# Optimization experiments

Hardware: AMD Instinct MI355X
Metric: run time of the kernel (lower is better)

Reference implementation:

```python
import jax, jax.numpy as jnp
import numpy as np

B, T, C_IN, CH, NRC, ED, NL, K = 16, 4096, 165, 256, 32, 64, 4, 512


def conv1x1(x, w, b):
    # x: [B,T,Cin], w: [Cout,Cin], b: [Cout]  (kernel-size-1 Conv1d == per-timestep matmul)
    return jnp.einsum('btc,oc->bto', x, w) + b


def resblock(x, wa, ba, wb, bb):
    h = jax.nn.relu(x)
    h = jax.nn.relu(conv1x1(h, wa, ba))
    h = conv1x1(h, wb, bb)
    return x + h


def quantize_level(res, embed):
    # res: [B,T,D], embed: [D,K]
    D = res.shape[-1]
    flat = res.reshape(-1, D)  # [N,D]
    dist = (flat * flat).sum(1, keepdims=True) - 2.0 * (flat @ embed) + (embed * embed).sum(0, keepdims=True)  # [N,K]
    ind = jnp.argmin(dist, axis=1)
    q = jnp.take(embed.T, ind, axis=0).reshape(res.shape)  # codebook gather
    diff = jnp.mean(jnp.square(jax.lax.stop_gradient(q) - res))
    q_st = res + jax.lax.stop_gradient(q - res)  # straight-through
    return q_st, diff


def _p(key, shape, fan_in):
    return jax.random.normal(key, shape, dtype=jnp.float32) / np.sqrt(fan_in)


def setup_inputs() -> dict:
    key = jax.random.key(0)
    ks = jax.random.split(key, 32)
    d = {
        'x': jax.random.normal(ks[0], (B, T, C_IN), dtype=jnp.float32),
        'enc_w1': _p(ks[1], (CH // 2, C_IN), C_IN), 'enc_b1': jnp.zeros((CH // 2,), jnp.float32),
        'enc_w2': _p(ks[2], (CH, CH // 2), CH // 2), 'enc_b2': jnp.zeros((CH,), jnp.float32),
        'enc_w3': _p(ks[3], (CH, CH), CH), 'enc_b3': jnp.zeros((CH,), jnp.float32),
        'enc_res_wa': _p(ks[4], (2, NRC, CH), CH), 'enc_res_ba': jnp.zeros((2, NRC), jnp.float32),
        'enc_res_wb': _p(ks[5], (2, CH, NRC), NRC), 'enc_res_bb': jnp.zeros((2, CH), jnp.float32),
        # quantize_conv: Conv(256->64)
        'q_w': _p(ks[6], (ED, CH), CH), 'q_b': jnp.zeros((ED,), jnp.float32),
        # 4 codebooks [D,K] (torch.randn init)
        'embeds': jax.random.normal(ks[7], (NL, ED, K), dtype=jnp.float32),
        'dec_w1': _p(ks[8], (CH, ED), ED), 'dec_b1': jnp.zeros((CH,), jnp.float32),
        'dec_res_wa': _p(ks[9], (2, NRC, CH), CH), 'dec_res_ba': jnp.zeros((2, NRC), jnp.float32),
        'dec_res_wb': _p(ks[10], (2, CH, NRC), NRC), 'dec_res_bb': jnp.zeros((2, CH), jnp.float32),
        'dec_w2': _p(ks[11], (CH // 2, CH), CH), 'dec_b2': jnp.zeros((CH // 2,), jnp.float32),
        'dec_w3': _p(ks[12], (C_IN, CH // 2), CH // 2), 'dec_b3': jnp.zeros((C_IN,), jnp.float32),
    }
    return d


def reference(x, enc_w1, enc_b1, enc_w2, enc_b2, enc_w3, enc_b3,
              enc_res_wa, enc_res_ba, enc_res_wb, enc_res_bb,
              q_w, q_b, embeds,
              dec_w1, dec_b1, dec_res_wa, dec_res_ba, dec_res_wb, dec_res_bb,
              dec_w2, dec_b2, dec_w3, dec_b3):
    # work entirely in [B,T,C] layout (transposes in the torch code cancel)
    h = jax.nn.relu(conv1x1(x, enc_w1, enc_b1))
    h = jax.nn.relu(conv1x1(h, enc_w2, enc_b2))
    h = conv1x1(h, enc_w3, enc_b3)
    for i in range(2):
        h = resblock(h, enc_res_wa[i], enc_res_ba[i], enc_res_wb[i], enc_res_bb[i])
    h = jax.nn.relu(h)
    quant = conv1x1(h, q_w, q_b)  # [B,T,64]

    residual = quant
    diffs = []
    main_q = None
    for i in range(NL):
        q, d = quantize_level(residual, embeds[i])
        diffs.append(d)
        residual = residual - q
        if i == 0:
            main_q = q
    diff = jnp.mean(jnp.stack(diffs))[None]  # shape [1]

    d = conv1x1(main_q, dec_w1, dec_b1)
    for i in range(2):
        d = resblock(d, dec_res_wa[i], dec_res_ba[i], dec_res_wb[i], dec_res_bb[i])
    d = jax.nn.relu(d)
    d = jax.nn.relu(conv1x1(d, dec_w2, dec_b2))
    d = conv1x1(d, dec_w3, dec_b3)  # [B,T,165]
    return d, diff
```

## Files before the change

### kernel.cpp

```cpp
#include <hip/hip_runtime.h>

#define NROWS 65536
#define SB 256

__device__ __forceinline__ float frelu(float v) { return fmaxf(v, 0.f); }

#define OFF_WT1   0
#define OFF_WT2   21504
#define OFF_WT3   54272
#define OFF_WTQ   119808
#define OFF_WTD1  136192
#define OFF_WTD2  152576
#define OFF_WTD3  185344
#define OFF_WAPE  218112
#define OFF_WBTE  234496
#define OFF_WAPD  250880
#define OFF_WBTD  267264
#define OFF_ETG   283648
#define OFF_EN2   414720
#define OFF_DSUM  416768
#define PREP_N    416769

__global__ void prep_k(const float* __restrict__ ew1, const float* __restrict__ ew2,
                       const float* __restrict__ ew3, const float* __restrict__ qw,
                       const float* __restrict__ dw1, const float* __restrict__ dw2,
                       const float* __restrict__ dw3, const float* __restrict__ ewa,
                       const float* __restrict__ ewb, const float* __restrict__ dwa,
                       const float* __restrict__ dwb, const float* __restrict__ embeds,
                       float* __restrict__ W) {
  int idx = blockIdx.x * 256 + threadIdx.x;
  if (idx < 21504) {
    int k = idx >> 7, o = idx & 127;
    W[OFF_WT1 + idx] = (k < 165) ? ew1[o * 165 + k] : 0.f;
    return;
  }
  idx -= 21504;
  if (idx < 32768) {
    int k = idx >> 8, o = idx & 255;
    W[OFF_WT2 + idx] = ew2[o * 128 + k];
    return;
  }
  idx -= 32768;
  if (idx < 65536) {
    int k = idx >> 8, o = idx & 255;
    W[OFF_WT3 + idx] = ew3[o * 256 + k];
    return;
  }
  idx -= 65536;
  if (idx < 16384) {
    int k = idx >> 6, o = idx & 63;
    W[OFF_WTQ + idx] = qw[o * 256 + k];
    return;
  }
  idx -= 16384;
  if (idx < 16384) {
    int k = idx >> 8, o = idx & 255;
    W[OFF_WTD1 + idx] = dw1[o * 64 + k];
    return;
  }
  idx -= 16384;
  if (idx < 32768) {
    int k = idx >> 7, o = idx & 127;
    W[OFF_WTD2 + idx] = dw2[o * 256 + k];
    return;
  }
  idx -= 32768;
  if (idx < 32768) {
    int k = idx >> 8, o = idx & 255;
    W[OFF_WTD3 + idx] = (o < 165) ? dw3[o * 128 + k] : 0.f;
    return;
  }
  idx -= 32768;
  if (idx < 16384) {
    int l = idx >> 13, rem = idx & 8191;
    int k4 = rem >> 7, rem2 = rem & 127, o = rem2 >> 2, kk = rem2 & 3;
    W[OFF_WAPE + idx] = ewa[l * 8192 + o * 256 + k4 * 4 + kk];
    return;
  }
  idx -= 16384;
  if (idx < 16384) {
    int l = idx >> 13, rem = idx & 8191;
    int k = rem >> 8, o = rem & 255;
    W[OFF_WBTE + idx] = ewb[l * 8192 + o * 32 + k];
    return;
  }
  idx -= 16384;
  if (idx < 16384) {
    int l = idx >> 13, rem = idx & 8191;
    int k4 = rem >> 7, rem2 = rem & 127, o = rem2 >> 2, kk = rem2 & 3;
    W[OFF_WAPD + idx] = dwa[l * 8192 + o * 256 + k4 * 4 + kk];
    return;
  }
  idx -= 16384;
  if (idx < 16384) {
    int l = idx >> 13, rem = idx & 8191;
    int k = rem >> 8, o = rem & 255;
    W[OFF_WBTD + idx] = dwb[l * 8192 + o * 32 + k];
    return;
  }
  idx -= 16384;
  if (idx < 131072) {
    int d = idx & 63, k = (idx >> 6) & 511, l = idx >> 15;
    W[OFF_ETG + idx] = embeds[(l * 64 + d) * 512 + k];
    return;
  }
  idx -= 131072;
  if (idx < 2048) {
    int l = idx >> 9, k = idx & 511;
    float s = 0.f;
    for (int d = 0; d < 64; ++d) {
      float e = embeds[(l * 64 + d) * 512 + k];
      s = fmaf(e, e, s);
    }
    W[OFF_EN2 + idx] = s;
    return;
  }
  idx -= 2048;
  if (idx == 0) W[OFF_DSUM] = 0.f;
}

template <int CIN, int CINP, int COUT, int CP, int INSTRIDE, int OUTSTRIDE, bool RELU_IN,
          bool RELU_OUT>
__global__ __launch_bounds__(256, 4) void conv2_k(const float* in, const float* __restrict__ wT,
                                                  const float* __restrict__ b, float* out) {
  constexpr int COUTP = 64 * CP;
  constexpr bool GUARD = (COUT != COUTP);
  typedef float vCP __attribute__((ext_vector_type(CP)));
  __shared__ float xs[32][CINP];
  const int tid = threadIdx.x, lane = tid & 63, wv = tid >> 6;
  const long row0 = (long)blockIdx.x * 32;

  for (int i = tid; i < 32 * CINP; i += 256) {
    const int r = i / CINP, c = i % CINP;
    float v = (CIN == CINP || c < CIN) ? in[(row0 + r) * (long)INSTRIDE + c] : 0.f;
    if (RELU_IN) v = frelu(v);
    xs[r][c] = v;
  }
  __syncthreads();

  float acc[8][CP];
#pragma unroll
  for (int i = 0; i < 8; ++i)
#pragma unroll
    for (int j = 0; j < CP; ++j) acc[i][j] = 0.f;

  const float* wbase = wT + lane * CP;
#pragma unroll 4
  for (int k0 = 0; k0 < CINP; k0 += 4) {
    vCP wk[4];
#pragma unroll
    for (int kk = 0; kk < 4; ++kk) wk[kk] = *(const vCP*)(wbase + (k0 + kk) * COUTP);
#pragma unroll
    for (int rj = 0; rj < 8; ++rj) {
      const float4 x = *(const float4*)(&xs[wv * 8 + rj][k0]);
#pragma unroll
      for (int j = 0; j < CP; ++j) {
        acc[rj][j] = fmaf(x.x, wk[0][j], acc[rj][j]);
        acc[rj][j] = fmaf(x.y, wk[1][j], acc[rj][j]);
        acc[rj][j] = fmaf(x.z, wk[2][j], acc[rj][j]);
        acc[rj][j] = fmaf(x.w, wk[3][j], acc[rj][j]);
      }
    }
  }

  float bias[CP];
#pragma unroll
  for (int j = 0; j < CP; ++j) {
    const int o = lane * CP + j;
    bias[j] = (!GUARD || o < COUT) ? b[o] : 0.f;
  }
#pragma unroll
  for (int rj = 0; rj < 8; ++rj) {
    const long rbase = (row0 + wv * 8 + rj) * (long)OUTSTRIDE;
    if constexpr (!GUARD) {
      vCP v;
#pragma unroll
      for (int j = 0; j < CP; ++j) {
        const float t = acc[rj][j] + bias[j];
        v[j] = RELU_OUT ? frelu(t) : t;
      }
      *(vCP*)(out + rbase + lane * CP) = v;
    } else {
#pragma unroll
      for (int j = 0; j < CP; ++j) {
        const int o = lane * CP + j;
        if (o < COUT) {
          const float t = acc[rj][j] + bias[j];
          out[rbase + o] = RELU_OUT ? frelu(t) : t;
        }
      }
    }
  }
}

__global__ __launch_bounds__(512, 4) void resblock_pair_k(
    float* xbuf, const float* __restrict__ waP, const float* __restrict__ ba,
    const float* __restrict__ wbT, const float* __restrict__ bb) {
  __shared__ float wls[8192];
  __shared__ float ts[64][36];
  const int tid = threadIdx.x, lane = tid & 63, wv = tid >> 6;
  const long row0 = (long)blockIdx.x * 64;
  const int o32 = lane & 31, rh = lane >> 5;

  for (int li = 0; li < 2; ++li) {
    __syncthreads();
    for (int i = tid; i < 8192; i += 512) wls[i] = waP[li * 8192 + i];
    __syncthreads();

    {
      float a0 = 0.f, a1 = 0.f, a2 = 0.f, a3 = 0.f;
      const float* xrow = xbuf + (row0 + wv * 8 + rh * 4) * (long)SB;
#pragma unroll 4
      for (int k0 = 0; k0 < 256; k0 += 4) {
        const float4 wq = *(const float4*)(&wls[k0 * 32 + o32 * 4]);
        const float4 x0 = *(const float4*)(xrow + 0 * SB + k0);
        const float4 x1 = *(const float4*)(xrow + 1 * SB + k0);
        const float4 x2 = *(const float4*)(xrow + 2 * SB + k0);
        const float4 x3 = *(const float4*)(xrow + 3 * SB + k0);
        a0 = fmaf(frelu(x0.x), wq.x, a0);
        a0 = fmaf(frelu(x0.y), wq.y, a0);
        a0 = fmaf(frelu(x0.z), wq.z, a0);
        a0 = fmaf(frelu(x0.w), wq.w, a0);
        a1 = fmaf(frelu(x1.x), wq.x, a1);
        a1 = fmaf(frelu(x1.y), wq.y, a1);
        a1 = fmaf(frelu(x1.z), wq.z, a1);
        a1 = fmaf(frelu(x1.w), wq.w, a1);
        a2 = fmaf(frelu(x2.x), wq.x, a2);
        a2 = fmaf(frelu(x2.y), wq.y, a2);
        a2 = fmaf(frelu(x2.z), wq.z, a2);
        a2 = fmaf(frelu(x2.w), wq.w, a2);
        a3 = fmaf(frelu(x3.x), wq.x, a3);
        a3 = fmaf(frelu(x3.y), wq.y, a3);
        a3 = fmaf(frelu(x3.z), wq.z, a3);
        a3 = fmaf(frelu(x3.w), wq.w, a3);
      }
      const float bal = ba[li * 32 + o32];
      const int rB = wv * 8 + rh * 4;
      ts[rB + 0][o32] = frelu(a0 + bal);
      ts[rB + 1][o32] = frelu(a1 + bal);
      ts[rB + 2][o32] = frelu(a2 + bal);
      ts[rB + 3][o32] = frelu(a3 + bal);
    }

    __syncthreads();
    for (int i = tid; i < 8192; i += 512) wls[i] = wbT[li * 8192 + i];
    __syncthreads();

    float acc2[8][4];
#pragma unroll
    for (int i = 0; i < 8; ++i)
#pragma unroll
      for (int j = 0; j < 4; ++j) acc2[i][j] = 0.f;

#pragma unroll
    for (int k0 = 0; k0 < 32; k0 += 4) {
      const float4 wk0 = *(const float4*)(&wls[(k0 + 0) * 256 + lane * 4]);
      const float4 wk1 = *(const float4*)(&wls[(k0 + 1) * 256 + lane * 4]);
      const float4 wk2 = *(const float4*)(&wls[(k0 + 2) * 256 + lane * 4]);
      const float4 wk3 = *(const float4*)(&wls[(k0 + 3) * 256 + lane * 4]);
#pragma unroll
      for (int rj = 0; rj < 8; ++rj) {
        const float4 t4 = *(const float4*)(&ts[wv * 8 + rj][k0]);
        acc2[rj][0] = fmaf(t4.x, wk0.x, acc2[rj][0]);
        acc2[rj][1] = fmaf(t4.x, wk0.y, acc2[rj][1]);
        acc2[rj][2] = fmaf(t4.x, wk0.z, acc2[rj][2]);
        acc2[rj][3] = fmaf(t4.x, wk0.w, acc2[rj][3]);
        acc2[rj][0] = fmaf(t4.y, wk1.x, acc2[rj][0]);
        acc2[rj][1] = fmaf(t4.y, wk1.y, acc2[rj][1]);
        acc2[rj][2] = fmaf(t4.y, wk1.z, acc2[rj][2]);
        acc2[rj][3] = fmaf(t4.y, wk1.w, acc2[rj][3]);
        acc2[rj][0] = fmaf(t4.z, wk2.x, acc2[rj][0]);
        acc2[rj][1] = fmaf(t4.z, wk2.y, acc2[rj][1]);
        acc2[rj][2] = fmaf(t4.z, wk2.z, acc2[rj][2]);
        acc2[rj][3] = fmaf(t4.z, wk2.w, acc2[rj][3]);
        acc2[rj][0] = fmaf(t4.w, wk3.x, acc2[rj][0]);
        acc2[rj][1] = fmaf(t4.w, wk3.y, acc2[rj][1]);
        acc2[rj][2] = fmaf(t4.w, wk3.z, acc2[rj][2]);
        acc2[rj][3] = fmaf(t4.w, wk3.w, acc2[rj][3]);
      }
    }
    const float4 bbv = *(const float4*)(bb + li * 256 + lane * 4);
#pragma unroll
    for (int rj = 0; rj < 8; ++rj) {
      float* xp = xbuf + (row0 + wv * 8 + rj) * (long)SB + lane * 4;
      const float4 xv = *(const float4*)xp;
      float4 nv;
      nv.x = xv.x + acc2[rj][0] + bbv.x;
      nv.y = xv.y + acc2[rj][1] + bbv.y;
      nv.z = xv.z + acc2[rj][2] + bbv.z;
      nv.w = xv.w + acc2[rj][3] + bbv.w;
      *(float4*)xp = nv;
    }
  }
}

__global__ __launch_bounds__(256, 4) void vq_k(float* buf, const float* __restrict__ embeds,
                                               const float* __restrict__ en2,
                                               const float* __restrict__ etg,
                                               float* __restrict__ dsum) {
  __shared__ float resL[32][68];
  const int tid = threadIdx.x;
  const int lane = tid & 63;
  const int wv = tid >> 6;
  const long row0 = (long)blockIdx.x * 32;

  for (int rj = 0; rj < 8; ++rj) {
    const int r = wv * 8 + rj;
    resL[r][lane] = buf[(row0 + r) * (long)SB + lane];
  }

  float dloc = 0.f;

  for (int l = 0; l < 4; ++l) {
    float best[8];
    int bk[8];
#pragma unroll
    for (int i = 0; i < 8; ++i) {
      best[i] = 3.4e38f;
      bk[i] = 0;
    }

    for (int kc = 0; kc < 2; ++kc) {
      float acc[8][4];
#pragma unroll
      for (int i = 0; i < 8; ++i)
#pragma unroll
        for (int j = 0; j < 4; ++j) acc[i][j] = 0.f;

      const float* eb = embeds + ((long)l << 15) + (kc << 8) + lane * 4;
#pragma unroll 2
      for (int dq = 0; dq < 16; ++dq) {
        float4 x4[8];
#pragma unroll
        for (int rj = 0; rj < 8; ++rj) x4[rj] = *(const float4*)(&resL[wv * 8 + rj][dq * 4]);
#pragma unroll
        for (int dd = 0; dd < 4; ++dd) {
          const float4 e4 = *(const float4*)(eb + ((dq * 4 + dd) << 9));
#pragma unroll
          for (int rj = 0; rj < 8; ++rj) {
            const float xv = dd == 0 ? x4[rj].x : dd == 1 ? x4[rj].y : dd == 2 ? x4[rj].z : x4[rj].w;
            acc[rj][0] = fmaf(xv, e4.x, acc[rj][0]);
            acc[rj][1] = fmaf(xv, e4.y, acc[rj][1]);
            acc[rj][2] = fmaf(xv, e4.z, acc[rj][2]);
            acc[rj][3] = fmaf(xv, e4.w, acc[rj][3]);
          }
        }
      }

      const float4 e2 = *(const float4*)(en2 + l * 512 + kc * 256 + lane * 4);
#pragma unroll
      for (int rj = 0; rj < 8; ++rj) {
#pragma unroll
        for (int j = 0; j < 4; ++j) {
          const float ev = j == 0 ? e2.x : j == 1 ? e2.y : j == 2 ? e2.z : e2.w;
          const float s = fmaf(-2.f, acc[rj][j], ev);
          const int k = kc * 256 + lane * 4 + j;
          if (s < best[rj]) {
            best[rj] = s;
            bk[rj] = k;
          }
        }
      }
    }

#pragma unroll
    for (int rj = 0; rj < 8; ++rj) {
      float bv = best[rj];
      int bi = bk[rj];
#pragma unroll
      for (int m = 1; m < 64; m <<= 1) {
        const float ov = __shfl_xor(bv, m, 64);
        const int ok = __shfl_xor(bi, m, 64);
        if (ov < bv || (ov == bv && ok < bi)) {
          bv = ov;
          bi = ok;
        }
      }
      bk[rj] = bi;
    }

#pragma unroll
    for (int rj = 0; rj < 8; ++rj) {
      const int r = wv * 8 + rj;
      const float q = etg[((long)((l << 9) + bk[rj])) * 64 + lane];
      const float res = resL[r][lane];
      const float t = q - res;
      const float qst = res + t;
      dloc = fmaf(t, t, dloc);
      resL[r][lane] = res - qst;
      if (l == 0) buf[(row0 + r) * (long)SB + lane] = qst;
    }
  }

#pragma unroll
  for (int m = 1; m < 64; m <<= 1) dloc += __shfl_xor(dloc, m, 64);
  if (lane == 0) atomicAdd(dsum, dloc);
}

__global__ void finalize_k(const float* __restrict__ dsum, float* __restrict__ out) {
  if (threadIdx.x == 0 && blockIdx.x == 0)
    out[0] = *dsum * (1.0f / (4.0f * 65536.0f * 64.0f));
}

extern "C" void kernel_launch(void* const* d_in, const int* in_sizes, int n_in, void* d_out,
                              int out_size, void* d_ws, size_t ws_size, hipStream_t stream) {
  (void)in_sizes; (void)n_in; (void)out_size; (void)ws_size;
  const float* x = (const float*)d_in[0];
  const float* enc_w1 = (const float*)d_in[1];
  const float* enc_b1 = (const float*)d_in[2];
  const float* enc_w2 = (const float*)d_in[3];
  const float* enc_b2 = (const float*)d_in[4];
  const float* enc_w3 = (const float*)d_in[5];
  const float* enc_b3 = (const float*)d_in[6];
  const float* enc_res_wa = (const float*)d_in[7];
  const float* enc_res_ba = (const float*)d_in[8];
  const float* enc_res_wb = (const float*)d_in[9];
  const float* enc_res_bb = (const float*)d_in[10];
  const float* q_w = (const float*)d_in[11];
  const float* q_b = (const float*)d_in[12];
  const float* embeds = (const float*)d_in[13];
  const float* dec_w1 = (const float*)d_in[14];
  const float* dec_b1 = (const float*)d_in[15];
  const float* dec_res_wa = (const float*)d_in[16];
  const float* dec_res_ba = (const float*)d_in[17];
  const float* dec_res_wb = (const float*)d_in[18];
  const float* dec_res_bb = (const float*)d_in[19];
  const float* dec_w2 = (const float*)d_in[20];
  const float* dec_b2 = (const float*)d_in[21];
  const float* dec_w3 = (const float*)d_in[22];
  const float* dec_b3 = (const float*)d_in[23];

  float* ws = (float*)d_ws;
  float* buf = ws;
  float* W = ws + (long)NROWS * SB;

  float* dout = (float*)d_out;

  prep_k<<<(PREP_N + 255) / 256, 256, 0, stream>>>(enc_w1, enc_w2, enc_w3, q_w, dec_w1, dec_w2,
                                                   dec_w3, enc_res_wa, enc_res_wb, dec_res_wa,
                                                   dec_res_wb, embeds, W);

  const int GB = NROWS / 32;
  const int GR = NROWS / 64;

  conv2_k<165, 168, 128, 2, 165, SB, false, true><<<GB, 256, 0, stream>>>(x, W + OFF_WT1, enc_b1, buf);
  conv2_k<128, 128, 256, 4, SB, SB, false, true><<<GB, 256, 0, stream>>>(buf, W + OFF_WT2, enc_b2, buf);
  conv2_k<256, 256, 256, 4, SB, SB, false, false><<<GB, 256, 0, stream>>>(buf, W + OFF_WT3, enc_b3, buf);
  resblock_pair_k<<<GR, 512, 0, stream>>>(buf, W + OFF_WAPE, enc_res_ba, W + OFF_WBTE, enc_res_bb);
  conv2_k<256, 256, 64, 1, SB, SB, true, false><<<GB, 256, 0, stream>>>(buf, W + OFF_WTQ, q_b, buf);

  vq_k<<<GB, 256, 0, stream>>>(buf, embeds, W + OFF_EN2, W + OFF_ETG, W + OFF_DSUM);

  conv2_k<64, 64, 256, 4, SB, SB, false, false><<<GB, 256, 0, stream>>>(buf, W + OFF_WTD1, dec_b1, buf);
  resblock_pair_k<<<GR, 512, 0, stream>>>(buf, W + OFF_WAPD, dec_res_ba, W + OFF_WBTD, dec_res_bb);
  conv2_k<256, 256, 128, 2, SB, SB, true, true><<<GB, 256, 0, stream>>>(buf, W + OFF_WTD2, dec_b2, buf);
  conv2_k<128, 128, 165, 4, SB, 165, false, false><<<GB, 256, 0, stream>>>(buf, W + OFF_WTD3, dec_b3, dout);

  finalize_k<<<1, 64, 0, stream>>>(W + OFF_DSUM, dout + (long)NROWS * 165);
}
```

Baseline: 1.234 ms.

## Enlarge VQ register tile to 16 rows x 8 codes per thread

The VQ distance kernel now gives each block 64 rows instead of 32. Each thread computes a 16-row by 8-code accumulator tile covering all 512 codes in a single pass, instead of two 256-code passes over an 8x4 tile. This means more FMAs per codebook load and per LDS read, and the two-pass loop with its repeated residual reloads goes away. In exchange, the 128 accumulators raise register pressure: launch bounds drop to 2 blocks per CU and the grid halves, which lowers occupancy and may cause spills.

```diff
diff --git a/kernel.cpp b/kernel.cpp
--- a/kernel.cpp
+++ b/kernel.cpp
@@ -294,77 +294,115 @@
   }
 }
 
-__global__ __launch_bounds__(256, 4) void vq_k(float* buf, const float* __restrict__ embeds,
+__global__ __launch_bounds__(256, 2) void vq_k(float* buf, const float* __restrict__ embeds,
                                                const float* __restrict__ en2,
                                                const float* __restrict__ etg,
                                                float* __restrict__ dsum) {
-  __shared__ float resL[32][68];
+  __shared__ float resL[64][68];
   const int tid = threadIdx.x;
   const int lane = tid & 63;
   const int wv = tid >> 6;
-  const long row0 = (long)blockIdx.x * 32;
-
-  for (int rj = 0; rj < 8; ++rj) {
-    const int r = wv * 8 + rj;
+  const long row0 = (long)blockIdx.x * 64;
+
+#pragma unroll
+  for (int rj = 0; rj < 16; ++rj) {
+    const int r = wv * 16 + rj;
     resL[r][lane] = buf[(row0 + r) * (long)SB + lane];
   }
 
   float dloc = 0.f;
 
   for (int l = 0; l < 4; ++l) {
-    float best[8];
-    int bk[8];
-#pragma unroll
-    for (int i = 0; i < 8; ++i) {
+    float best[16];
+    int bk[16];
+#pragma unroll
+    for (int i = 0; i < 16; ++i) {
       best[i] = 3.4e38f;
       bk[i] = 0;
     }
 
-    for (int kc = 0; kc < 2; ++kc) {
-      float acc[8][4];
-#pragma unroll
-      for (int i = 0; i < 8; ++i)
-#pragma unroll
-        for (int j = 0; j < 4; ++j) acc[i][j] = 0.f;
-
-      const float* eb = embeds + ((long)l << 15) + (kc << 8) + lane * 4;
+    float acc[16][8];
+#pragma unroll
+    for (int i = 0; i < 16; ++i)
+#pragma unroll
+      for (int j = 0; j < 8; ++j) acc[i][j] = 0.f;
+
+    const float* eb0 = embeds + ((long)l << 15) + lane * 4;
+    const float* eb1 = eb0 + 256;
+
 #pragma unroll 2
-      for (int dq = 0; dq < 16; ++dq) {
-        float4 x4[8];
-#pragma unroll
-        for (int rj = 0; rj < 8; ++rj) x4[rj] = *(const float4*)(&resL[wv * 8 + rj][dq * 4]);
-#pragma unroll
-        for (int dd = 0; dd < 4; ++dd) {
-          const float4 e4 = *(const float4*)(eb + ((dq * 4 + dd) << 9));
-#pragma unroll
-          for (int rj = 0; rj < 8; ++rj) {
-            const float xv = dd == 0 ? x4[rj].x : dd == 1 ? x4[rj].y : dd == 2 ? x4[rj].z : x4[rj].w;
-            acc[rj][0] = fmaf(xv, e4.x, acc[rj][0]);
-            acc[rj][1] = fmaf(xv, e4.y, acc[rj][1]);
-            acc[rj][2] = fmaf(xv, e4.z, acc[rj][2]);
-            acc[rj][3] = fmaf(xv, e4.w, acc[rj][3]);
-          }
-        }
-      }
-
-      const float4 e2 = *(const float4*)(en2 + l * 512 + kc * 256 + lane * 4);
-#pragma unroll
-      for (int rj = 0; rj < 8; ++rj) {
-#pragma unroll
-        for (int j = 0; j < 4; ++j) {
-          const float ev = j == 0 ? e2.x : j == 1 ? e2.y : j == 2 ? e2.z : e2.w;
-          const float s = fmaf(-2.f, acc[rj][j], ev);
-          const int k = kc * 256 + lane * 4 + j;
-          if (s < best[rj]) {
-            best[rj] = s;
-            bk[rj] = k;
-          }
-        }
-      }
-    }
-
-#pragma unroll
-    for (int rj = 0; rj < 8; ++rj) {
+    for (int dq = 0; dq < 16; ++dq) {
+      const float4 ea0 = *(const float4*)(eb0 + ((dq * 4 + 0) << 9));
+      const float4 ea1 = *(const float4*)(eb0 + ((dq * 4 + 1) << 9));
+      const float4 ea2 = *(const float4*)(eb0 + ((dq * 4 + 2) << 9));
+      const float4 ea3 = *(const float4*)(eb0 + ((dq * 4 + 3) << 9));
+      const float4 eb0v = *(const float4*)(eb1 + ((dq * 4 + 0) << 9));
+      const float4 eb1v = *(const float4*)(eb1 + ((dq * 4 + 1) << 9));
+      const float4 eb2v = *(const float4*)(eb1 + ((dq * 4 + 2) << 9));
+      const float4 eb3v = *(const float4*)(eb1 + ((dq * 4 + 3) << 9));
+#pragma unroll
+      for (int rj = 0; rj < 16; ++rj) {
+        const float4 x = *(const float4*)(&resL[wv * 16 + rj][dq * 4]);
+        acc[rj][0] = fmaf(x.x, ea0.x, acc[rj][0]);
+        acc[rj][1] = fmaf(x.x, ea0.y, acc[rj][1]);
+        acc[rj][2] = fmaf(x.x, ea0.z, acc[rj][2]);
+        acc[rj][3] = fmaf(x.x, ea0.w, acc[rj][3]);
+        acc[rj][4] = fmaf(x.x, eb0v.x, acc[rj][4]);
+        acc[rj][5] = fmaf(x.x, eb0v.y, acc[rj][5]);
+        acc[rj][6] = fmaf(x.x, eb0v.z, acc[rj][6]);
+        acc[rj][7] = fmaf(x.x, eb0v.w, acc[rj][7]);
+        acc[rj][0] = fmaf(x.y, ea1.x, acc[rj][0]);
+        acc[rj][1] = fmaf(x.y, ea1.y, acc[rj][1]);
+        acc[rj][2] = fmaf(x.y, ea1.z, acc[rj][2]);
+        acc[rj][3] = fmaf(x.y, ea1.w, acc[rj][3]);
+        acc[rj][4] = fmaf(x.y, eb1v.x, acc[rj][4]);
+        acc[rj][5] = fmaf(x.y, eb1v.y, acc[rj][5]);
+        acc[rj][6] = fmaf(x.y, eb1v.z, acc[rj][6]);
+        acc[rj][7] = fmaf(x.y, eb1v.w, acc[rj][7]);
+        acc[rj][0] = fmaf(x.z, ea2.x, acc[rj][0]);
+        acc[rj][1] = fmaf(x.z, ea2.y, acc[rj][1]);
+        acc[rj][2] = fmaf(x.z, ea2.z, acc[rj][2]);
+        acc[rj][3] = fmaf(x.z, ea2.w, acc[rj][3]);
+        acc[rj][4] = fmaf(x.z, eb2v.x, acc[rj][4]);
+        acc[rj][5] = fmaf(x.z, eb2v.y, acc[rj][5]);
+        acc[rj][6] = fmaf(x.z, eb2v.z, acc[rj][6]);
+        acc[rj][7] = fmaf(x.z, eb2v.w, acc[rj][7]);
+        acc[rj][0] = fmaf(x.w, ea3.x, acc[rj][0]);
+        acc[rj][1] = fmaf(x.w, ea3.y, acc[rj][1]);
+        acc[rj][2] = fmaf(x.w, ea3.z, acc[rj][2]);
+        acc[rj][3] = fmaf(x.w, ea3.w, acc[rj][3]);
+        acc[rj][4] = fmaf(x.w, eb3v.x, acc[rj][4]);
+        acc[rj][5] = fmaf(x.w, eb3v.y, acc[rj][5]);
+        acc[rj][6] = fmaf(x.w, eb3v.z, acc[rj][6]);
+        acc[rj][7] = fmaf(x.w, eb3v.w, acc[rj][7]);
+      }
+    }
+
+    const float4 e2a = *(const float4*)(en2 + l * 512 + lane * 4);
+    const float4 e2b = *(const float4*)(en2 + l * 512 + 256 + lane * 4);
+#pragma unroll
+    for (int rj = 0; rj < 16; ++rj) {
+      float s;
+      s = fmaf(-2.f, acc[rj][0], e2a.x);
+      if (s < best[rj]) { best[rj] = s; bk[rj] = lane * 4 + 0; }
+      s = fmaf(-2.f, acc[rj][1], e2a.y);
+      if (s < best[rj]) { best[rj] = s; bk[rj] = lane * 4 + 1; }
+      s = fmaf(-2.f, acc[rj][2], e2a.z);
+      if (s < best[rj]) { best[rj] = s; bk[rj] = lane * 4 + 2; }
+      s = fmaf(-2.f, acc[rj][3], e2a.w);
+      if (s < best[rj]) { best[rj] = s; bk[rj] = lane * 4 + 3; }
+      s = fmaf(-2.f, acc[rj][4], e2b.x);
+      if (s < best[rj]) { best[rj] = s; bk[rj] = 256 + lane * 4 + 0; }
+      s = fmaf(-2.f, acc[rj][5], e2b.y);
+      if (s < best[rj]) { best[rj] = s; bk[rj] = 256 + lane * 4 + 1; }
+      s = fmaf(-2.f, acc[rj][6], e2b.z);
+      if (s < best[rj]) { best[rj] = s; bk[rj] = 256 + lane * 4 + 2; }
+      s = fmaf(-2.f, acc[rj][7], e2b.w);
+      if (s < best[rj]) { best[rj] = s; bk[rj] = 256 + lane * 4 + 3; }
+    }
+
+#pragma unroll
+    for (int rj = 0; rj < 16; ++rj) {
       float bv = best[rj];
       int bi = bk[rj];
 #pragma unroll
@@ -380,8 +418,8 @@
     }
 
 #pragma unroll
-    for (int rj = 0; rj < 8; ++rj) {
-      const int r = wv * 8 + rj;
+    for (int rj = 0; rj < 16; ++rj) {
+      const int r = wv * 16 + rj;
       const float q = etg[((long)((l << 9) + bk[rj])) * 64 + lane];
       const float res = resL[r][lane];
       const float t = q - res;
@@ -449,7 +487,7 @@
   resblock_pair_k<<<GR, 512, 0, stream>>>(buf, W + OFF_WAPE, enc_res_ba, W + OFF_WBTE, enc_res_bb);
   conv2_k<256, 256, 64, 1, SB, SB, true, false><<<GB, 256, 0, stream>>>(buf, W + OFF_WTQ, q_b, buf);
 
-  vq_k<<<GB, 256, 0, stream>>>(buf, embeds, W + OFF_EN2, W + OFF_ETG, W + OFF_DSUM);
+  vq_k<<<GR, 256, 0, stream>>>(buf, embeds, W + OFF_EN2, W + OFF_ETG, W + OFF_DSUM);
 
   conv2_k<64, 64, 256, 4, SB, SB, false, false><<<GB, 256, 0, stream>>>(buf, W + OFF_WTD1, dec_b1, buf);
   resblock_pair_k<<<GR, 512, 0, stream>>>(buf, W + OFF_WAPD, dec_res_ba, W + OFF_WBTD, dec_res_bb);
```

Measured after the change: 1.565 ms. 1.27x slower.
